# Kernel optimization log

Measured on AMD Instinct MI355X. Metric: run time of the kernel, lower is better.

## Reference

```python
import jax, jax.numpy as jnp
import numpy as np

BETA = 25.0  # torch nn.Softplus(beta=25.0)

def softplus_b(z):
    return jax.nn.softplus(BETA * z) / BETA

def setup_inputs() -> dict:
    key = jax.random.key(0)
    ks = jax.random.split(key, 9)
    B, H = 16384, 512
    def lin_init(kw, kb, out_f, in_f):
        bound = 1.0 / np.sqrt(in_f)
        W = jax.random.uniform(kw, (out_f, in_f), jnp.float32, -bound, bound)
        b = jax.random.uniform(kb, (out_f,), jnp.float32, -bound, bound)
        return W, b
    W0, b0 = lin_init(ks[1], ks[2], H, 4)
    W1, b1 = lin_init(ks[3], ks[4], H, H)
    W2, b2 = lin_init(ks[5], ks[6], H, H)
    W3, b3 = lin_init(ks[7], ks[8], 5, H)
    x = jax.random.normal(ks[0], (B, 4), jnp.float32)
    return {"x": x, "W0": W0, "b0": b0, "W1": W1, "b1": b1,
            "W2": W2, "b2": b2, "W3": W3, "b3": b3}

def reference(x, W0, b0, W1, b1, W2, b2, W3, b3):
    def net(z):  # (4,) -> (5,)
        h = softplus_b(W0 @ z + b0)
        h = softplus_b(W1 @ h + b1)
        h = softplus_b(W2 @ h + b2)
        return W3 @ h + b3

    def A_matrix(z):  # antisymmetrized Jacobian of first 4 outputs, (4,4)
        J = jax.jacrev(lambda p: net(p)[:4])(z)
        return J - J.T

    def point_trace(z):
        # T[i,j,k] = d A[i,j] / d z[k]; torch einsum('...ii') -> sum_j T[i,j,j]
        T = jax.jacfwd(A_matrix)(z)  # (4,4,4)
        return jnp.einsum('ijj->i', T)  # (4,)

    trace = jax.vmap(point_trace)(x)          # (B,4)
    u = jax.vmap(net)(x)                      # (B,5)
    return jnp.concatenate([trace, u[:, 4:5]], axis=1)  # (B,5)
```

## Files before the change

kernel.cpp:

```cpp
#include <hip/hip_runtime.h>
#include <math.h>

#define HDIM 512
#define NCH 16
#define BETA 25.0f
#define KV 1536
#define NKH 48

typedef unsigned short ushort_t;
typedef __attribute__((ext_vector_type(8))) short short8;
typedef __attribute__((ext_vector_type(4))) float f32x4;

__device__ __forceinline__ ushort_t f2bf(float f) {
    unsigned u = __float_as_uint(f);
    unsigned r = (u + 0x7fff + ((u >> 16) & 1)) >> 16;
    return (ushort_t)r;
}
__device__ __forceinline__ float bf2f(ushort_t b) {
    return __uint_as_float(((unsigned)b) << 16);
}
__device__ __forceinline__ void split_bf(float v, ushort_t& hi, ushort_t& lo) {
    hi = f2bf(v);
    lo = f2bf(v - bf2f(hi));
}

__device__ __forceinline__ void softplus_jet(float v, float& phi, float& s, float& pp) {
    float y = BETA * v;
    float e = expf(-fabsf(y));
    float inv = 1.0f / (1.0f + e);
    s = (y >= 0.0f) ? inv : e * inv;
    phi = (fmaxf(y, 0.0f) + log1pf(e)) * (1.0f / BETA);
    pp = BETA * s * (1.0f - s);
}

__device__ __forceinline__ void gl_lds16(const void* g, void* l) {
    __builtin_amdgcn_global_load_lds(
        (const __attribute__((address_space(1))) unsigned int*)g,
        (__attribute__((address_space(3))) unsigned int*)l, 16, 0, 0);
}

__global__ __launch_bounds__(256) void layer0_jet(
    const float* __restrict__ x, const float* __restrict__ W0,
    const float* __restrict__ b0, ushort_t* __restrict__ A0)
{
    __shared__ ushort_t sm[16 * 1024];
    int p = blockIdx.x, tid = threadIdx.x;
    float4 z = *reinterpret_cast<const float4*>(&x[p * 4]);
#pragma unroll
    for (int half = 0; half < 2; ++half) {
        int n = half * 256 + tid;
        float4 w = *reinterpret_cast<const float4*>(&W0[n * 4]);
        float v = fmaf(w.x, z.x, fmaf(w.y, z.y, fmaf(w.z, z.z, fmaf(w.w, z.w, b0[n]))));
        float phi, s, pp;
        softplus_jet(v, phi, s, pp);
        float wa[4] = {w.x, w.y, w.z, w.w};
        float o[16];
        o[0] = phi;
#pragma unroll
        for (int a = 0; a < 4; ++a) o[1 + a] = s * wa[a];
        int idx = 5;
#pragma unroll
        for (int a = 0; a < 4; ++a)
#pragma unroll
            for (int b = a; b < 4; ++b) { o[idx] = pp * wa[a] * wa[b]; ++idx; }
        o[15] = 0.0f;
#pragma unroll
        for (int c = 0; c < 16; ++c) {
            ushort_t hb, lb;
            split_bf(o[c], hb, lb);
            sm[c * 1024 + n] = hb;
            sm[c * 1024 + 512 + n] = lb;
        }
    }
    __syncthreads();
    uint4* d4 = reinterpret_cast<uint4*>(A0 + (size_t)p * 16 * 1024);
    const uint4* s4 = reinterpret_cast<const uint4*>(sm);
#pragma unroll
    for (int i = 0; i < 8; ++i) d4[tid + 256 * i] = s4[tid + 256 * i];
}

template<int EPI>
__global__ __launch_bounds__(512, 2) void gemm_jet8(
    const ushort_t* __restrict__ Ag, const ushort_t* __restrict__ BT,
    const float* __restrict__ bias, ushort_t* __restrict__ Anext,
    float* __restrict__ Sout)
{
    __shared__ char smem[131072];
    ushort_t* Asl = (ushort_t*)smem;
    ushort_t* Bsl = (ushort_t*)(smem + 65536);
    float*    epi = (float*)smem;

    const int tid = threadIdx.x;
    const int wave = tid >> 6, lane = tid & 63;
    const int wr = wave >> 2, wc = wave & 3;

    int nwg = gridDim.x, bid = blockIdx.x;
    int q = nwg >> 3, r = nwg & 7;
    int xcd = bid & 7, i8 = bid >> 3;
    int logical = (xcd < r ? xcd * (q + 1) : r * (q + 1) + (xcd - r) * q) + i8;
    const int mt = logical >> 1;
    const int m0 = mt * 256;
    const int n0 = (logical & 1) * 256;

    const int s_w2 = wave * 2;
    const int s_row = lane >> 2;
    const int s_c  = (((lane & 3) - ((lane >> 3) & 3)) & 3) * 8;

    f32x4 acc[8][4] = {};

    auto stageA = [&](int g) {
        if (g >= NKH) g -= NKH;
        const int slot = g & 3;
        int k0 = g * 32;
        int ka = (k0 < 512) ? k0 : k0 - 512;
#pragma unroll
        for (int rr = 0; rr < 2; ++rr) {
            int row = (s_w2 + rr) * 16 + s_row;
            gl_lds16(Ag + (size_t)(m0 + row) * 1024 + ka + s_c,
                     Asl + slot * 8192 + (s_w2 + rr) * 512);
        }
    };
    auto stageB = [&](int g) {
        if (g >= NKH) g -= NKH;
        const int slot = g & 3;
        int k0 = g * 32;
#pragma unroll
        for (int rr = 0; rr < 2; ++rr) {
            int row = (s_w2 + rr) * 16 + s_row;
            gl_lds16(BT + (size_t)(n0 + row) * KV + k0 + s_c,
                     Bsl + slot * 8192 + (s_w2 + rr) * 512);
        }
    };

    const int rA = lane & 15;
    const int rd = rA * 32 + ((((lane >> 4) + (rA >> 1)) & 3) * 8);

    stageA(0); stageB(0); stageA(1); stageB(1); stageA(2); stageB(2);
    asm volatile("s_waitcnt vmcnt(8)" ::: "memory");
    __builtin_amdgcn_s_barrier();
    asm volatile("" ::: "memory");

    short8 afA[4], afB[4], bfr[4];
#pragma unroll
    for (int mi = 0; mi < 4; ++mi)
        afA[mi] = *(const short8*)&Asl[(wr * 128 + mi * 16) * 32 + rd];
#pragma unroll
    for (int ni = 0; ni < 4; ++ni)
        bfr[ni] = *(const short8*)&Bsl[(wc * 64 + ni * 16) * 32 + rd];

#pragma unroll 4
    for (int g = 0; g < NKH; ++g) {
        const int slot = g & 3;
        const int slot1 = (g + 1) & 3;
        {
#pragma unroll
            for (int mi = 0; mi < 4; ++mi)
                afB[mi] = *(const short8*)&Asl[slot * 8192 + (wr * 128 + 64 + mi * 16) * 32 + rd];
            stageA(g + 3);
            asm volatile("s_waitcnt vmcnt(6)" ::: "memory");
            __builtin_amdgcn_s_barrier();
            __builtin_amdgcn_s_setprio(1);
#pragma unroll
            for (int mi = 0; mi < 4; ++mi)
#pragma unroll
                for (int ni = 0; ni < 4; ++ni)
                    acc[mi][ni] = __builtin_amdgcn_mfma_f32_16x16x32_bf16(
                        afA[mi], bfr[ni], acc[mi][ni], 0, 0, 0);
            __builtin_amdgcn_s_setprio(0);
            asm volatile("" ::: "memory");
            __builtin_amdgcn_s_barrier();
            asm volatile("" ::: "memory");
        }
        {
#pragma unroll
            for (int mi = 0; mi < 4; ++mi)
                afA[mi] = *(const short8*)&Asl[slot1 * 8192 + (wr * 128 + mi * 16) * 32 + rd];
            stageB(g + 3);
            asm volatile("s_waitcnt vmcnt(6)" ::: "memory");
            __builtin_amdgcn_s_barrier();
            __builtin_amdgcn_s_setprio(1);
#pragma unroll
            for (int mi = 0; mi < 4; ++mi)
#pragma unroll
                for (int ni = 0; ni < 4; ++ni)
                    acc[4 + mi][ni] = __builtin_amdgcn_mfma_f32_16x16x32_bf16(
                        afB[mi], bfr[ni], acc[4 + mi][ni], 0, 0, 0);
            __builtin_amdgcn_s_setprio(0);
#pragma unroll
            for (int ni = 0; ni < 4; ++ni)
                bfr[ni] = *(const short8*)&Bsl[slot1 * 8192 + (wc * 64 + ni * 16) * 32 + rd];
            asm volatile("" ::: "memory");
            __builtin_amdgcn_s_barrier();
            asm volatile("" ::: "memory");
        }
    }

    asm volatile("s_waitcnt vmcnt(0) lgkmcnt(0)" ::: "memory");
    __builtin_amdgcn_s_barrier();
    asm volatile("" ::: "memory");

    const int pl = lane & 15, ph = lane >> 4;
    const int wxor = (ph & 1) << 4;
#pragma unroll
    for (int h = 0; h < 2; ++h) {
        if (h) { asm volatile("" ::: "memory"); __builtin_amdgcn_s_barrier(); }
        if (wr == h) {
#pragma unroll
            for (int am = 0; am < 8; ++am)
#pragma unroll
                for (int ni = 0; ni < 4; ++ni)
#pragma unroll
                    for (int rr = 0; rr < 4; ++rr)
                        epi[(am * 16 + ph * 4 + rr) * 256 + ((wc * 64 + ni * 16 + pl) ^ wxor)] = acc[am][ni][rr];
        }
        asm volatile("" ::: "memory");
        __builtin_amdgcn_s_barrier();
        asm volatile("" ::: "memory");
#pragma unroll
        for (int rep = 0; rep < 4; ++rep) {
            int idx = rep * 512 + tid;
            int n = idx & 255, pq = idx >> 8;
            const float* vp = &epi[pq * 16 * 256];
            float v[15];
#pragma unroll
            for (int c = 0; c < 15; ++c) v[c] = vp[c * 256 + (n ^ (((c >> 2) & 1) << 4))];
            float val = v[0] + bias[n0 + n];
            float phi, s, pp;
            softplus_jet(val, phi, s, pp);
            float o[16];
            o[0] = phi;
            float d[4];
#pragma unroll
            for (int a = 0; a < 4; ++a) { d[a] = v[1 + a]; o[1 + a] = s * d[a]; }
            int ix = 5;
#pragma unroll
            for (int a = 0; a < 4; ++a)
#pragma unroll
                for (int b = a; b < 4; ++b) { o[ix] = pp * d[a] * d[b] + s * v[ix]; ++ix; }
            o[15] = 0.0f;
            size_t prow = (size_t)mt * 16 + h * 8 + pq;
            if (EPI == 1) {
                size_t rb = prow * 16 * 1024;
#pragma unroll
                for (int c = 0; c < 16; ++c) {
                    ushort_t hb, lb;
                    split_bf(o[c], hb, lb);
                    Anext[rb + (size_t)c * 1024 + n0 + n] = hb;
                    Anext[rb + (size_t)c * 1024 + 512 + n0 + n] = lb;
                }
            } else {
                float4* op = reinterpret_cast<float4*>(Sout + ((size_t)prow * 512 + n0 + n) * 16);
#pragma unroll
                for (int qq = 0; qq < 4; ++qq)
                    op[qq] = make_float4(o[4*qq], o[4*qq+1], o[4*qq+2], o[4*qq+3]);
            }
        }
    }
}

__global__ __launch_bounds__(256) void trace_kernel(
    const float* __restrict__ Sin, const float* __restrict__ W3,
    const float* __restrict__ b3, float* __restrict__ out, int npts)
{
    int wave = threadIdx.x >> 6;
    int lane = threadIdx.x & 63;
    int p = blockIdx.x * 4 + wave;
    if (p >= npts) return;
    const float* sp = Sin + (size_t)p * (HDIM * NCH);

    float hu[4][10];
#pragma unroll
    for (int m = 0; m < 4; ++m)
#pragma unroll
        for (int qq = 0; qq < 10; ++qq) hu[m][qq] = 0.0f;
    float u4 = 0.0f;

    for (int kk = 0; kk < 8; ++kk) {
        int k = kk * 64 + lane;
        const float* sk = sp + k * NCH;
        float4 s0 = *reinterpret_cast<const float4*>(&sk[0]);
        float4 s1 = *reinterpret_cast<const float4*>(&sk[4]);
        float4 s2 = *reinterpret_cast<const float4*>(&sk[8]);
        float4 s3 = *reinterpret_cast<const float4*>(&sk[12]);
        float hv[10] = {s1.y,s1.z,s1.w, s2.x,s2.y,s2.z,s2.w, s3.x,s3.y,s3.z};
        float w3m[5];
#pragma unroll
        for (int m = 0; m < 5; ++m) w3m[m] = W3[m * HDIM + k];
        u4 = fmaf(w3m[4], s0.x, u4);
#pragma unroll
        for (int m = 0; m < 4; ++m)
#pragma unroll
            for (int qq = 0; qq < 10; ++qq) hu[m][qq] = fmaf(w3m[m], hv[qq], hu[m][qq]);
    }

#pragma unroll
    for (int off = 32; off > 0; off >>= 1) {
#pragma unroll
        for (int m = 0; m < 4; ++m)
#pragma unroll
            for (int qq = 0; qq < 10; ++qq) hu[m][qq] += __shfl_xor(hu[m][qq], off, 64);
        u4 += __shfl_xor(u4, off, 64);
    }

    if (lane == 0) {
        const int Pm[4][4] = {{0,1,2,3},{1,4,5,6},{2,5,7,8},{3,6,8,9}};
        const int Pd[4] = {0, 4, 7, 9};
#pragma unroll
        for (int i = 0; i < 4; ++i) {
            float t1 = hu[i][Pd[0]] + hu[i][Pd[1]] + hu[i][Pd[2]] + hu[i][Pd[3]];
            float t2 = hu[0][Pm[0][i]] + hu[1][Pm[1][i]] + hu[2][Pm[2][i]] + hu[3][Pm[3][i]];
            out[p * 5 + i] = t1 - t2;
        }
        out[p * 5 + 4] = u4 + b3[4];
    }
}

__global__ void prep_B(const float* __restrict__ W1, const float* __restrict__ W2,
                       ushort_t* __restrict__ BT1, ushort_t* __restrict__ BT2)
{
    int tid = blockIdx.x * 256 + threadIdx.x;
    int l = tid >> 18;
    int i = tid & 262143;
    int n = i >> 9, k = i & 511;
    const float* W = l ? W2 : W1;
    ushort_t* BT = l ? BT2 : BT1;
    float v = W[i];
    ushort_t hb, lb;
    split_bf(v, hb, lb);
    size_t rr = (size_t)n * KV;
    BT[rr + k] = hb;
    BT[rr + 512 + k] = lb;
    BT[rr + 1024 + k] = hb;
}

extern "C" void kernel_launch(void* const* d_in, const int* in_sizes, int n_in,
                              void* d_out, int out_size, void* d_ws, size_t ws_size,
                              hipStream_t stream)
{
    const float* x  = (const float*)d_in[0];
    const float* W0 = (const float*)d_in[1];
    const float* b0 = (const float*)d_in[2];
    const float* W1 = (const float*)d_in[3];
    const float* b1 = (const float*)d_in[4];
    const float* W2 = (const float*)d_in[5];
    const float* b2 = (const float*)d_in[6];
    const float* W3 = (const float*)d_in[7];
    const float* b3 = (const float*)d_in[8];
    float* out = (float*)d_out;

    int B = in_sizes[0] / 4;

    ushort_t* BT1 = (ushort_t*)d_ws;
    ushort_t* BT2 = BT1 + 512 * KV;
    char* bufbase = (char*)(BT2 + 512 * KV);

    size_t avail = ws_size - 2ull * 512 * KV * sizeof(ushort_t);
    size_t per_pt = 2ull * 32768;
    int Pc = (int)(avail / per_pt) & ~15;
    if (Pc > 16384) Pc = 16384;
    if (Pc < 16) Pc = 16;

    ushort_t* A0 = (ushort_t*)bufbase;
    ushort_t* A1 = (ushort_t*)(bufbase + (size_t)Pc * 32768);
    float* S2 = (float*)A0;

    prep_B<<<2048, 256, 0, stream>>>(W1, W2, BT1, BT2);

    for (int base = 0; base < B; base += Pc) {
        int np = (B - base < Pc) ? (B - base) : Pc;
        layer0_jet<<<np, 256, 0, stream>>>(x + (size_t)base * 4, W0, b0, A0);
        int nwg = (np / 16) * 2;
        gemm_jet8<1><<<nwg, 512, 0, stream>>>(A0, BT1, b1, A1, nullptr);
        gemm_jet8<2><<<nwg, 512, 0, stream>>>(A1, BT2, b2, nullptr, S2);
        trace_kernel<<<(np + 3) / 4, 256, 0, stream>>>(S2, W3, b3, out + (size_t)base * 5, np);
    }
}
```

Baseline: 1.316 ms.

## Shrink GEMM tile to 256x128 with 4 waves and triple-buffered LDS

The jet GEMM moves from 512-thread 256x256 tiles to 256-thread 256x128 tiles with four waves, doubling the workgroup count, and LDS drops from 128KB to 72KB with a 3-slot pipeline instead of 4. The weight matrix no longer stores a duplicated hi copy (KV 1536 -> 1024). The k-schedule is reordered so the A-hi slice is reused against both B-hi and B-lo, which keeps the same three split-bf16 products. The intent is better occupancy and less weight traffic, at the cost of more A re-reads across N tiles and a shallower prefetch.

```diff
diff --git a/kernel.cpp b/kernel.cpp
--- a/kernel.cpp
+++ b/kernel.cpp
@@ -4,7 +4,6 @@
 #define HDIM 512
 #define NCH 16
 #define BETA 25.0f
-#define KV 1536
 #define NKH 48
 
 typedef unsigned short ushort_t;
@@ -80,63 +79,61 @@
 }
 
 template<int EPI>
-__global__ __launch_bounds__(512, 2) void gemm_jet8(
+__global__ __launch_bounds__(256, 2) void gemm_jet8(
     const ushort_t* __restrict__ Ag, const ushort_t* __restrict__ BT,
     const float* __restrict__ bias, ushort_t* __restrict__ Anext,
     float* __restrict__ Sout)
 {
-    __shared__ char smem[131072];
+    __shared__ char smem[73728];
     ushort_t* Asl = (ushort_t*)smem;
-    ushort_t* Bsl = (ushort_t*)(smem + 65536);
+    ushort_t* Bsl = (ushort_t*)(smem + 49152);
     float*    epi = (float*)smem;
 
     const int tid = threadIdx.x;
     const int wave = tid >> 6, lane = tid & 63;
-    const int wr = wave >> 2, wc = wave & 3;
+    const int wr = wave >> 1, wc = wave & 1;
 
     int nwg = gridDim.x, bid = blockIdx.x;
     int q = nwg >> 3, r = nwg & 7;
     int xcd = bid & 7, i8 = bid >> 3;
     int logical = (xcd < r ? xcd * (q + 1) : r * (q + 1) + (xcd - r) * q) + i8;
-    const int mt = logical >> 1;
+    const int mt = logical >> 2;
     const int m0 = mt * 256;
-    const int n0 = (logical & 1) * 256;
-
-    const int s_w2 = wave * 2;
-    const int s_row = lane >> 2;
-    const int s_c  = (((lane & 3) - ((lane >> 3) & 3)) & 3) * 8;
+    const int n0 = (logical & 3) * 128;
+
+    const int s_c = (((lane & 3) - ((lane >> 3) & 3)) & 3) * 8;
 
     f32x4 acc[8][4] = {};
 
-    auto stageA = [&](int g) {
-        if (g >= NKH) g -= NKH;
-        const int slot = g & 3;
-        int k0 = g * 32;
-        int ka = (k0 < 512) ? k0 : k0 - 512;
+    auto kaof = [](int g) { return (g < 32) ? (g >> 1) * 32 : 512 + (g - 32) * 32; };
+    auto kbof = [](int g) { return (g < 32) ? ((g & 1) << 9) + (g >> 1) * 32 : (g - 32) * 32; };
+
+    auto stageA = [&](int g, int slot) {
+        if (g >= NKH) g = 0;
+        int ka = kaof(g);
+#pragma unroll
+        for (int rr = 0; rr < 4; ++rr) {
+            int row = rr * 64 + wave * 16 + (lane >> 2);
+            gl_lds16(Ag + (size_t)(m0 + row) * 1024 + ka + s_c,
+                     Asl + slot * 8192 + rr * 2048 + wave * 512);
+        }
+    };
+    auto stageB = [&](int g, int slot) {
+        if (g >= NKH) g = 0;
+        int kb = kbof(g);
 #pragma unroll
         for (int rr = 0; rr < 2; ++rr) {
-            int row = (s_w2 + rr) * 16 + s_row;
-            gl_lds16(Ag + (size_t)(m0 + row) * 1024 + ka + s_c,
-                     Asl + slot * 8192 + (s_w2 + rr) * 512);
-        }
-    };
-    auto stageB = [&](int g) {
-        if (g >= NKH) g -= NKH;
-        const int slot = g & 3;
-        int k0 = g * 32;
-#pragma unroll
-        for (int rr = 0; rr < 2; ++rr) {
-            int row = (s_w2 + rr) * 16 + s_row;
-            gl_lds16(BT + (size_t)(n0 + row) * KV + k0 + s_c,
-                     Bsl + slot * 8192 + (s_w2 + rr) * 512);
+            int row = rr * 64 + wave * 16 + (lane >> 2);
+            gl_lds16(BT + (size_t)(n0 + row) * 1024 + kb + s_c,
+                     Bsl + slot * 4096 + rr * 2048 + wave * 512);
         }
     };
 
     const int rA = lane & 15;
     const int rd = rA * 32 + ((((lane >> 4) + (rA >> 1)) & 3) * 8);
 
-    stageA(0); stageB(0); stageA(1); stageB(1); stageA(2); stageB(2);
-    asm volatile("s_waitcnt vmcnt(8)" ::: "memory");
+    stageA(0, 0); stageB(0, 0); stageA(1, 1); stageB(1, 1);
+    asm volatile("s_waitcnt vmcnt(6)" ::: "memory");
     __builtin_amdgcn_s_barrier();
     asm volatile("" ::: "memory");
 
@@ -148,16 +145,18 @@
     for (int ni = 0; ni < 4; ++ni)
         bfr[ni] = *(const short8*)&Bsl[(wc * 64 + ni * 16) * 32 + rd];
 
-#pragma unroll 4
-    for (int g = 0; g < NKH; ++g) {
-        const int slot = g & 3;
-        const int slot1 = (g + 1) & 3;
-        {
+    for (int gj = 0; gj < 16; ++gj) {
+#pragma unroll
+        for (int u = 0; u < 3; ++u) {
+            const int g = gj * 3 + u;
+            const int s  = u;
+            const int s1 = (u + 1) % 3;
+            const int s2 = (u + 2) % 3;
 #pragma unroll
             for (int mi = 0; mi < 4; ++mi)
-                afB[mi] = *(const short8*)&Asl[slot * 8192 + (wr * 128 + 64 + mi * 16) * 32 + rd];
-            stageA(g + 3);
-            asm volatile("s_waitcnt vmcnt(6)" ::: "memory");
+                afB[mi] = *(const short8*)&Asl[s * 8192 + (wr * 128 + 64 + mi * 16) * 32 + rd];
+            stageA(g + 2, s2);
+            asm volatile("s_waitcnt vmcnt(4)" ::: "memory");
             __builtin_amdgcn_s_barrier();
             __builtin_amdgcn_s_setprio(1);
 #pragma unroll
@@ -170,13 +169,10 @@
             asm volatile("" ::: "memory");
             __builtin_amdgcn_s_barrier();
             asm volatile("" ::: "memory");
-        }
-        {
 #pragma unroll
             for (int mi = 0; mi < 4; ++mi)
-                afA[mi] = *(const short8*)&Asl[slot1 * 8192 + (wr * 128 + mi * 16) * 32 + rd];
-            stageB(g + 3);
-            asm volatile("s_waitcnt vmcnt(6)" ::: "memory");
+                afA[mi] = *(const short8*)&Asl[s1 * 8192 + (wr * 128 + mi * 16) * 32 + rd];
+            stageB(g + 2, s2);
             __builtin_amdgcn_s_barrier();
             __builtin_amdgcn_s_setprio(1);
 #pragma unroll
@@ -188,7 +184,7 @@
             __builtin_amdgcn_s_setprio(0);
 #pragma unroll
             for (int ni = 0; ni < 4; ++ni)
-                bfr[ni] = *(const short8*)&Bsl[slot1 * 8192 + (wc * 64 + ni * 16) * 32 + rd];
+                bfr[ni] = *(const short8*)&Bsl[s1 * 4096 + (wc * 64 + ni * 16) * 32 + rd];
             asm volatile("" ::: "memory");
             __builtin_amdgcn_s_barrier();
             asm volatile("" ::: "memory");
@@ -202,28 +198,29 @@
     const int pl = lane & 15, ph = lane >> 4;
     const int wxor = (ph & 1) << 4;
 #pragma unroll
-    for (int h = 0; h < 2; ++h) {
+    for (int h = 0; h < 4; ++h) {
         if (h) { asm volatile("" ::: "memory"); __builtin_amdgcn_s_barrier(); }
-        if (wr == h) {
-#pragma unroll
-            for (int am = 0; am < 8; ++am)
+        if (wr == (h >> 1)) {
+            const int ab = (h & 1) * 4;
+#pragma unroll
+            for (int lm = 0; lm < 4; ++lm)
 #pragma unroll
                 for (int ni = 0; ni < 4; ++ni)
 #pragma unroll
                     for (int rr = 0; rr < 4; ++rr)
-                        epi[(am * 16 + ph * 4 + rr) * 256 + ((wc * 64 + ni * 16 + pl) ^ wxor)] = acc[am][ni][rr];
+                        epi[(lm * 16 + ph * 4 + rr) * 128 + ((wc * 64 + ni * 16 + pl) ^ wxor)] = acc[ab + lm][ni][rr];
         }
         asm volatile("" ::: "memory");
         __builtin_amdgcn_s_barrier();
         asm volatile("" ::: "memory");
 #pragma unroll
-        for (int rep = 0; rep < 4; ++rep) {
-            int idx = rep * 512 + tid;
-            int n = idx & 255, pq = idx >> 8;
-            const float* vp = &epi[pq * 16 * 256];
+        for (int rep = 0; rep < 2; ++rep) {
+            int idx = rep * 256 + tid;
+            int n = idx & 127, pq = idx >> 7;
+            const float* vp = &epi[pq * 16 * 128];
             float v[15];
 #pragma unroll
-            for (int c = 0; c < 15; ++c) v[c] = vp[c * 256 + (n ^ (((c >> 2) & 1) << 4))];
+            for (int c = 0; c < 15; ++c) v[c] = vp[c * 128 + (n ^ (((c >> 2) & 1) << 4))];
             float val = v[0] + bias[n0 + n];
             float phi, s, pp;
             softplus_jet(val, phi, s, pp);
@@ -238,7 +235,7 @@
 #pragma unroll
                 for (int b = a; b < 4; ++b) { o[ix] = pp * d[a] * d[b] + s * v[ix]; ++ix; }
             o[15] = 0.0f;
-            size_t prow = (size_t)mt * 16 + h * 8 + pq;
+            size_t prow = (size_t)mt * 16 + h * 4 + pq;
             if (EPI == 1) {
                 size_t rb = prow * 16 * 1024;
 #pragma unroll
@@ -327,10 +324,9 @@
     float v = W[i];
     ushort_t hb, lb;
     split_bf(v, hb, lb);
-    size_t rr = (size_t)n * KV;
+    size_t rr = (size_t)n * 1024;
     BT[rr + k] = hb;
     BT[rr + 512 + k] = lb;
-    BT[rr + 1024 + k] = hb;
 }
 
 extern "C" void kernel_launch(void* const* d_in, const int* in_sizes, int n_in,
@@ -351,10 +347,10 @@
     int B = in_sizes[0] / 4;
 
     ushort_t* BT1 = (ushort_t*)d_ws;
-    ushort_t* BT2 = BT1 + 512 * KV;
-    char* bufbase = (char*)(BT2 + 512 * KV);
-
-    size_t avail = ws_size - 2ull * 512 * KV * sizeof(ushort_t);
+    ushort_t* BT2 = BT1 + 512 * 1024;
+    char* bufbase = (char*)(BT2 + 512 * 1024);
+
+    size_t avail = ws_size - 2ull * 512 * 1024 * sizeof(ushort_t);
     size_t per_pt = 2ull * 32768;
     int Pc = (int)(avail / per_pt) & ~15;
     if (Pc > 16384) Pc = 16384;
@@ -369,9 +365,9 @@
     for (int base = 0; base < B; base += Pc) {
         int np = (B - base < Pc) ? (B - base) : Pc;
         layer0_jet<<<np, 256, 0, stream>>>(x + (size_t)base * 4, W0, b0, A0);
-        int nwg = (np / 16) * 2;
-        gemm_jet8<1><<<nwg, 512, 0, stream>>>(A0, BT1, b1, A1, nullptr);
-        gemm_jet8<2><<<nwg, 512, 0, stream>>>(A1, BT2, b2, nullptr, S2);
+        int nwg = (np / 16) * 4;
+        gemm_jet8<1><<<nwg, 256, 0, stream>>>(A0, BT1, b1, A1, nullptr);
+        gemm_jet8<2><<<nwg, 256, 0, stream>>>(A1, BT2, b2, nullptr, S2);
         trace_kernel<<<(np + 3) / 4, 256, 0, stream>>>(S2, W3, b3, out + (size_t)base * 5, np);
     }
 }
```

Result: no change. 1.327 ms (+0.9%).
